# Performance work log

Measured on AMD Instinct MI355X. Metric: run time of the kernel, lower is better.

Reference implementation:

```python
import jax, jax.numpy as jnp
import numpy as np

EPS_NORM = 1e-12
BN_EPS = 1e-5
TEMP = 0.07


def _l2norm(x, axis):
    n = jnp.sqrt(jnp.sum(x * x, axis=axis, keepdims=True))
    return x / jnp.maximum(n, EPS_NORM)


def _bn_eval(z, w, b):
    # inference-mode BatchNorm2d with running_mean=0, running_var=1
    s = w / jnp.sqrt(jnp.asarray(1.0 + BN_EPS, z.dtype))
    return z * s[None, :, None, None] + b[None, :, None, None]


def setup_inputs() -> dict:
    key = jax.random.key(0)
    ks = jax.random.split(key, 8)
    B, C, H, W = 16, 256, 64, 64
    KD, P = 128, 256
    x = jax.random.normal(ks[0], (B, C, H, W), jnp.float32)
    m_features = jax.random.normal(ks[1], (P, KD), jnp.float32)
    q_w = jax.random.normal(ks[2], (KD, C), jnp.float32) * 0.05
    k_w = jax.random.normal(ks[3], (KD, KD), jnp.float32) * 0.05
    v_w = jax.random.normal(ks[4], (KD, KD), jnp.float32) * 0.05
    o_w = jax.random.normal(ks[5], (C, KD), jnp.float32) * 0.05
    dw_w = jax.random.normal(ks[6], (C, 1, 3, 3), jnp.float32) * 0.1
    return {
        "x": x, "m_features": m_features,
        "q_w": q_w, "q_b": jnp.zeros((KD,), jnp.float32),
        "k_w": k_w, "k_b": jnp.zeros((KD,), jnp.float32),
        "v_w": v_w, "v_b": jnp.zeros((KD,), jnp.float32),
        "o_w": o_w, "o_b": jnp.zeros((C,), jnp.float32),
        "dw_w": dw_w,
        "bn1_w": jnp.ones((C,), jnp.float32), "bn1_b": jnp.zeros((C,), jnp.float32),
        "bn2_w": jnp.ones((C,), jnp.float32), "bn2_b": jnp.zeros((C,), jnp.float32),
        "gamma": jnp.ones((C,), jnp.float32) * 1e-5,
    }


def reference(x, m_features, q_w, q_b, k_w, k_b, v_w, v_b, o_w, o_b,
              dw_w, bn1_w, bn1_b, bn2_w, bn2_b, gamma):
    B, C, H, W = x.shape
    KD = q_w.shape[0]
    residual = x
    # q_proj 1x1 conv -> [B,KD,H,W], L2-normalize over channel dim
    q = jnp.einsum('bchw,kc->bkhw', x, q_w) + q_b[None, :, None, None]
    q = _l2norm(q, axis=1)
    q = q.reshape(B, KD, H * W).transpose(0, 2, 1)  # [B, HW, KD]
    # k/v projections of memory bank [P, KD]
    k = _l2norm(m_features @ k_w.T + k_b, axis=-1)
    v = m_features @ v_w.T + v_b
    # fp32 attention with clamped logits
    q32, k32, v32 = q.astype(jnp.float32), k.astype(jnp.float32), v.astype(jnp.float32)
    logits = jnp.clip(jnp.einsum('bnd,pd->bnp', q32, k32) / TEMP, -30.0, 30.0)
    attn = jax.nn.softmax(logits, axis=-1)
    out = jnp.einsum('bnp,pd->bnd', attn, v32).astype(x.dtype)
    out = out.transpose(0, 2, 1).reshape(B, KD, H, W)
    # out_proj 1x1 conv -> [B,C,H,W]
    out = jnp.einsum('bkhw,ck->bchw', out, o_w) + o_b[None, :, None, None]
    # local branch: depthwise 3x3 conv + BN + exact GELU
    local = jax.lax.conv_general_dilated(
        out, dw_w, window_strides=(1, 1), padding='SAME',
        feature_group_count=C,
        dimension_numbers=('NCHW', 'OIHW', 'NCHW'))
    local = jax.nn.gelu(_bn_eval(local, bn1_w, bn1_b), approximate=False)
    out = out + local
    return _bn_eval(residual + out * gamma[None, :, None, None], bn2_w, bn2_b)
```

## Files before the change

### kernel.cpp

```cpp
#include <hip/hip_runtime.h>
#include <hip/hip_bf16.h>
#include <math.h>

#define B_ 16
#define C_ 256
#define H_ 64
#define W_ 64
#define KD_ 128
#define P_ 256
#define HW_ (H_ * W_)

typedef __bf16 bf16;
typedef bf16 bf16x8_t __attribute__((ext_vector_type(8)));
typedef bf16 bf16x4_t __attribute__((ext_vector_type(4)));
typedef float f32x4_t __attribute__((ext_vector_type(4)));
typedef float f32x16_t __attribute__((ext_vector_type(16)));
typedef unsigned char u8;

__device__ __forceinline__ unsigned cvt_pk_fp8_lo(float a, float b, unsigned old) {
#if __has_builtin(__builtin_amdgcn_cvt_pk_fp8_f32)
    return __builtin_amdgcn_cvt_pk_fp8_f32(a, b, old, false);
#else
    unsigned r = old;
    asm("v_cvt_pk_fp8_f32 %0, %1, %2" : "+v"(r) : "v"(a), "v"(b));
    return r;
#endif
}
__device__ __forceinline__ unsigned cvt_pk_fp8_hi(float a, float b, unsigned old) {
#if __has_builtin(__builtin_amdgcn_cvt_pk_fp8_f32)
    return __builtin_amdgcn_cvt_pk_fp8_f32(a, b, old, true);
#else
    unsigned r = old;
    asm("v_cvt_pk_fp8_f32 %0, %1, %2 op_sel:[0,0,1]" : "+v"(r) : "v"(a), "v"(b));
    return r;
#endif
}
__device__ __forceinline__ uint2 pack8_fp8(const float* f) {
    uint2 r;
    r.x = cvt_pk_fp8_hi(f[2], f[3], cvt_pk_fp8_lo(f[0], f[1], 0u));
    r.y = cvt_pk_fp8_hi(f[6], f[7], cvt_pk_fp8_lo(f[4], f[5], 0u));
    return r;
}

__global__ __launch_bounds__(128) void k_prep1(
    const float* __restrict__ m_feat,
    const float* __restrict__ k_w, const float* __restrict__ k_b,
    const float* __restrict__ v_w, const float* __restrict__ v_b,
    float* __restrict__ kn_f, float* __restrict__ v_f)
{
    const int p = blockIdx.x;
    const int j = threadIdx.x;
    __shared__ float msh[KD_];
    __shared__ float red[2];
    msh[j] = m_feat[p * KD_ + j];
    __syncthreads();

    float ka = k_b[j];
    float va = v_b[j];
#pragma unroll 4
    for (int d = 0; d < KD_; ++d) {
        const float m = msh[d];
        ka = fmaf(m, k_w[j * KD_ + d], ka);
        va = fmaf(m, v_w[j * KD_ + d], va);
    }
    float s = ka * ka;
#pragma unroll
    for (int o = 1; o < 64; o <<= 1) s += __shfl_xor(s, o);
    if ((j & 63) == 0) red[j >> 6] = s;
    __syncthreads();
    s = red[0] + red[1];
    const float inv = 1.0f / (0.07f * fmaxf(sqrtf(s), 1e-12f));
    kn_f[p * KD_ + j] = ka * inv;
    v_f[p * KD_ + j] = va;
}

__global__ __launch_bounds__(256) void k_prep23(
    const float* __restrict__ o_w, const float* __restrict__ v_f,
    const float* __restrict__ q_w, const float* __restrict__ kn_f,
    bf16* __restrict__ m2_bf, u8* __restrict__ qw8, u8* __restrict__ kn8)
{
    if (blockIdx.x < 256) {
        const int c = blockIdx.x;
        const int p = threadIdx.x;
        __shared__ float osh[KD_];
        if (p < KD_) osh[p] = o_w[c * KD_ + p];
        __syncthreads();
        float acc = 0.f;
#pragma unroll 4
        for (int k = 0; k < KD_; ++k) acc = fmaf(osh[k], v_f[p * KD_ + k], acc);
        const int mt = c >> 5, r = c & 31;
        const int ks = p >> 4, sub = (p >> 3) & 1, jj = p & 7;
        m2_bf[(((mt * 16 + ks) * 64) + sub * 32 + r) * 8 + jj] = (bf16)acc;
    } else {
        const int t = (blockIdx.x - 256) * 256 + threadIdx.x;
        float f[8];
        if (t < 4096) {
            const int lane = t & 63, g = t >> 6, mt = g >> 4, ks = g & 15;
            const int row = mt * 32 + (lane & 31), k0 = ks * 16 + (lane >> 5) * 8;
            const float* src = q_w + row * C_ + k0;
#pragma unroll
            for (int j = 0; j < 8; ++j) f[j] = src[j] * 16.0f;
            ((uint2*)qw8)[t] = pack8_fp8(f);
        } else {
            const int u = t - 4096;
            const int lane = u & 63, g = u >> 6, mt = g >> 3, ks = g & 7;
            const int row = mt * 32 + (lane & 31), k0 = ks * 16 + (lane >> 5) * 8;
            const float* src = kn_f + row * KD_ + k0;
#pragma unroll
            for (int j = 0; j < 8; ++j) f[j] = src[j];
            ((uint2*)kn8)[u] = pack8_fp8(f);
        }
    }
}

__global__ __launch_bounds__(512, 4) void k_attn(
    const float* __restrict__ x,
    const float* __restrict__ q_b, const float* __restrict__ o_b,
    const u8* __restrict__ qw8, const u8* __restrict__ kn8,
    const bf16* __restrict__ m2_bf, bf16* __restrict__ outf)
{
    __shared__ __align__(16) char lds[71680];
    char* const xs   = lds;
    char* const qbuf = lds + 32768;
    char* const ebuf = lds;
    float* ss_lds  = (float*)(lds + 65536);
    float* sum_lds = (float*)(lds + 67584);

    const int h0 = blockIdx.x * 2;
    const int b = blockIdx.y;
    const int tid = threadIdx.x;
    const int lane = tid & 63;
    const int wid = tid >> 6;
    const int l31 = lane & 31;
    const int kh  = lane >> 5;
    const int mtA = wid & 3, nhalf = wid >> 2;

    long kna[8];
#pragma unroll
    for (int ks = 0; ks < 8; ++ks)
        kna[ks] = *(const long*)(kn8 + ((wid * 8 + ks) * 64 + lane) * 8);

    {
        const int wq = tid & 15;
        const int cg = tid >> 4;
        const int c0 = cg * 8;
        const float* xrow = x + (size_t)b * C_ * HW_ + h0 * W_;
#pragma unroll
        for (int hl = 0; hl < 2; ++hl) {
            float v[8][4];
#pragma unroll
            for (int jj = 0; jj < 8; ++jj) {
                const f32x4_t t = *(const f32x4_t*)(xrow + (size_t)(c0 + jj) * HW_ + hl * W_ + wq * 4);
                v[jj][0] = t[0]; v[jj][1] = t[1]; v[jj][2] = t[2]; v[jj][3] = t[3];
            }
#pragma unroll
            for (int k = 0; k < 4; ++k) {
                const int pix = hl * 64 + wq * 4 + k;
                float f[8];
#pragma unroll
                for (int jj = 0; jj < 8; ++jj) f[jj] = v[jj][k];
                const int byte = pix * 256 + (c0 ^ ((pix & 31) << 3));
                *(uint2*)(xs + byte) = pack8_fp8(f);
            }
        }
    }
    __syncthreads();

    f32x16_t qacc[2];
#pragma unroll
    for (int nt = 0; nt < 2; ++nt)
#pragma unroll
        for (int i = 0; i < 16; ++i) qacc[nt][i] = 0.f;
#pragma unroll
    for (int ks = 0; ks < 16; ++ks) {
        const long a = *(const long*)(qw8 + ((mtA * 16 + ks) * 64 + lane) * 8);
#pragma unroll
        for (int nt = 0; nt < 2; ++nt) {
            const int pix = (nhalf * 2 + nt) * 32 + l31;
            const long bx = *(const long*)(xs + pix * 256 + ((ks * 16 + kh * 8) ^ (l31 << 3)));
            qacc[nt] = __builtin_amdgcn_mfma_f32_32x32x16_fp8_fp8(a, bx, qacc[nt], 0, 0, 0);
        }
    }
    {
        f32x4_t qbv[4];
#pragma unroll
        for (int g = 0; g < 4; ++g)
            qbv[g] = *(const f32x4_t*)(q_b + mtA * 32 + g * 8 + kh * 4);
#pragma unroll
        for (int nt = 0; nt < 2; ++nt) {
            const int pix = (nhalf * 2 + nt) * 32 + l31;
            float ssp = 0.f;
#pragma unroll
            for (int reg = 0; reg < 16; ++reg) {
                const int g = reg >> 2, i = reg & 3;
                const float qv = qacc[nt][reg] + 16.0f * qbv[g][i];
                qacc[nt][reg] = qv;
                ssp = fmaf(qv, qv, ssp);
            }
            ssp += __shfl_xor(ssp, 32);
            if (lane < 32) ss_lds[pix * 4 + mtA] = ssp;
#pragma unroll
            for (int g = 0; g < 4; ++g) {
                const unsigned qw_ = cvt_pk_fp8_hi(qacc[nt][g * 4 + 2], qacc[nt][g * 4 + 3],
                                    cvt_pk_fp8_lo(qacc[nt][g * 4 + 0], qacc[nt][g * 4 + 1], 0u));
                const int byte = pix * 128 + ((mtA * 32 + g * 8 + kh * 4) ^ ((l31 & 15) << 3));
                *(unsigned*)(qbuf + byte) = qw_;
            }
        }
    }
    __syncthreads();

    f32x16_t lacc[4];
#pragma unroll
    for (int nt = 0; nt < 4; ++nt)
#pragma unroll
        for (int i = 0; i < 16; ++i) lacc[nt][i] = 0.f;
#pragma unroll
    for (int ks = 0; ks < 8; ++ks) {
#pragma unroll
        for (int nt = 0; nt < 4; ++nt) {
            const int pix = nt * 32 + l31;
            const long bq = *(const long*)(qbuf + pix * 128 + ((ks * 16 + kh * 8) ^ ((l31 & 15) << 3)));
            lacc[nt] = __builtin_amdgcn_mfma_f32_32x32x16_fp8_fp8(kna[ks], bq, lacc[nt], 0, 0, 0);
        }
    }
    __syncthreads();

#pragma unroll
    for (int nt = 0; nt < 4; ++nt) {
        const int pix = nt * 32 + l31;
        const f32x4_t s4 = *(const f32x4_t*)(ss_lds + pix * 4);
        const float qinv = 1.0f / fmaxf(sqrtf(s4[0] + s4[1] + s4[2] + s4[3]), 1e-12f);
        float sm = 0.f;
#pragma unroll
        for (int reg = 0; reg < 16; ++reg) {
            const float e = __expf(lacc[nt][reg] * qinv);
            lacc[nt][reg] = e;
            sm += e;
        }
        sm += __shfl_xor(sm, 32);
        if (lane < 32) sum_lds[pix * 8 + wid] = sm;
#pragma unroll
        for (int g = 0; g < 4; ++g) {
            bf16x4_t e4;
#pragma unroll
            for (int i = 0; i < 4; ++i) e4[i] = (bf16)lacc[nt][g * 4 + i];
            const int byte = pix * 512 + (((wid * 32 + g * 8 + kh * 4) * 2) ^ (l31 << 4));
            *(bf16x4_t*)(ebuf + byte) = e4;
        }
    }
    __syncthreads();

    f32x16_t oacc[4];
#pragma unroll
    for (int nt = 0; nt < 4; ++nt)
#pragma unroll
        for (int i = 0; i < 16; ++i) oacc[nt][i] = 0.f;
#pragma unroll
    for (int ks = 0; ks < 16; ++ks) {
        const bf16x8_t a = *(const bf16x8_t*)(m2_bf + ((wid * 16 + ks) * 64 + lane) * 8);
#pragma unroll
        for (int nt = 0; nt < 4; ++nt) {
            const int pix = nt * 32 + l31;
            const bf16x8_t ba = *(const bf16x8_t*)(ebuf + pix * 512 + ((ks * 32 + kh * 16) ^ (l31 << 4)));
            oacc[nt] = __builtin_amdgcn_mfma_f32_32x32x16_bf16(a, ba, oacc[nt], 0, 0, 0);
        }
    }
    {
        f32x4_t obv[4];
#pragma unroll
        for (int g = 0; g < 4; ++g)
            obv[g] = *(const f32x4_t*)(o_b + wid * 32 + g * 8 + kh * 4);
        bf16* const obase = outf + (size_t)b * C_ * HW_ + h0 * W_;
#pragma unroll
        for (int nt = 0; nt < 4; ++nt) {
            const int pix = nt * 32 + l31;
            const f32x4_t sa = *(const f32x4_t*)(sum_lds + pix * 8);
            const f32x4_t sb = *(const f32x4_t*)(sum_lds + pix * 8 + 4);
            const float rs = 1.0f / ((sa[0] + sa[1] + sa[2] + sa[3]) +
                                     (sb[0] + sb[1] + sb[2] + sb[3]));
#pragma unroll
            for (int reg = 0; reg < 16; ++reg) {
                const int g = reg >> 2, i = reg & 3;
                const int c = wid * 32 + g * 8 + kh * 4 + i;
                obase[(size_t)c * HW_ + pix] = (bf16)fmaf(oacc[nt][reg], rs, obv[g][i]);
            }
        }
    }
}

__global__ __launch_bounds__(256) void k_post(
    const float* __restrict__ x, const bf16* __restrict__ outf,
    const float* __restrict__ dw_w,
    const float* __restrict__ bn1_w, const float* __restrict__ bn1_b,
    const float* __restrict__ bn2_w, const float* __restrict__ bn2_b,
    const float* __restrict__ gamma, float* __restrict__ y)
{
    __shared__ __align__(16) bf16 os[HW_];
    const int bc = blockIdx.x;
    const int c = bc & (C_ - 1);
    const int tid = threadIdx.x;

    const bf16* oc = outf + (size_t)bc * HW_;
#pragma unroll
    for (int it = 0; it < 2; ++it) {
        const int e = (it * 256 + tid) * 8;
        *(bf16x8_t*)&os[e] = *(const bf16x8_t*)&oc[e];
    }

    const float cbn = 0.99999500003750f;
    const float s1 = bn1_w[c] * cbn, b1 = bn1_b[c];
    const float s2 = bn2_w[c] * cbn, b2 = bn2_b[c];
    const float g = gamma[c];
    float kw[9];
#pragma unroll
    for (int j = 0; j < 9; ++j) kw[j] = dw_w[c * 9 + j];

    __syncthreads();

    const int w = tid & 63;
    const int h0 = (tid >> 6) * 16;

    float r0[3], r1[3], r2[3];
    auto ldrow = [&](int hh, float* r) {
        if ((unsigned)hh < (unsigned)H_) {
            r[1] = (float)os[hh * W_ + w];
            r[0] = (w > 0) ? (float)os[hh * W_ + w - 1] : 0.f;
            r[2] = (w < W_ - 1) ? (float)os[hh * W_ + w + 1] : 0.f;
        } else {
            r[0] = r[1] = r[2] = 0.f;
        }
    };
    ldrow(h0 - 1, r0);
    ldrow(h0, r1);

    const float* xc = x + (size_t)bc * HW_;
    float* yc = y + (size_t)bc * HW_;

#pragma unroll
    for (int i = 0; i < 16; ++i) {
        const int h = h0 + i;
        ldrow(h + 1, r2);
        float conv = kw[0] * r0[0];
        conv = fmaf(kw[1], r0[1], conv);
        conv = fmaf(kw[2], r0[2], conv);
        conv = fmaf(kw[3], r1[0], conv);
        conv = fmaf(kw[4], r1[1], conv);
        conv = fmaf(kw[5], r1[2], conv);
        conv = fmaf(kw[6], r2[0], conv);
        conv = fmaf(kw[7], r2[1], conv);
        conv = fmaf(kw[8], r2[2], conv);
        const float center = r1[1];
        const float t = fmaf(conv, s1, b1);
        const float lg = t / (1.0f + __expf(-1.702f * t));
        const int idx = h * W_ + w;
        yc[idx] = fmaf(center + lg, g, xc[idx]) * s2 + b2;
#pragma unroll
        for (int j = 0; j < 3; ++j) { r0[j] = r1[j]; r1[j] = r2[j]; }
    }
}

extern "C" void kernel_launch(void* const* d_in, const int* in_sizes, int n_in,
                              void* d_out, int out_size, void* d_ws, size_t ws_size,
                              hipStream_t stream)
{
    const float* x     = (const float*)d_in[0];
    const float* m_f   = (const float*)d_in[1];
    const float* q_w   = (const float*)d_in[2];
    const float* q_b   = (const float*)d_in[3];
    const float* k_w   = (const float*)d_in[4];
    const float* k_b   = (const float*)d_in[5];
    const float* v_w   = (const float*)d_in[6];
    const float* v_b   = (const float*)d_in[7];
    const float* o_w   = (const float*)d_in[8];
    const float* o_b   = (const float*)d_in[9];
    const float* dw_w  = (const float*)d_in[10];
    const float* bn1_w = (const float*)d_in[11];
    const float* bn1_b = (const float*)d_in[12];
    const float* bn2_w = (const float*)d_in[13];
    const float* bn2_b = (const float*)d_in[14];
    const float* gamma = (const float*)d_in[15];

    char* ws = (char*)d_ws;
    u8*    qw8   = (u8*)(ws);
    u8*    kn8   = (u8*)(ws + (32 << 10));
    bf16*  m2_bf = (bf16*)(ws + (64 << 10));
    bf16*  outf  = (bf16*)(ws + (384 << 10));
    float* kn_f  = (float*)(ws + (384 << 10));
    float* v_f   = (float*)(ws + (384 << 10) + (128 << 10));

    k_prep1<<<dim3(P_), dim3(128), 0, stream>>>(m_f, k_w, k_b, v_w, v_b,
                                                kn_f, v_f);
    k_prep23<<<dim3(288), dim3(256), 0, stream>>>(o_w, v_f, q_w, kn_f,
                                                  m2_bf, qw8, kn8);
    k_attn<<<dim3(H_ / 2, B_), dim3(512), 0, stream>>>(x, q_b, o_b, qw8, kn8,
                                                       m2_bf, outf);
    k_post<<<dim3(B_ * C_), dim3(256), 0, stream>>>(
        x, outf, dw_w, bn1_w, bn1_b, bn2_w, bn2_b, gamma, (float*)d_out);
}
```

Baseline: 75.35 us.

## Use FP8 for attention-value GEMM and halve attention tile to one row

The attention kernel now processes one image row (64 pixels) per 256-thread block instead of two rows per 512-thread block, which cuts LDS use from about 70KB to 27KB so more blocks can share a CU. The softmax probabilities and the fused o_w·v matrix are stored as FP8 (the latter scaled by 16) so the final GEMM uses FP8 MFMA instead of BF16. A per-pixel max is reduced across waves and subtracted, with a fixed offset, to keep the exponentials in FP8 range. This adds an extra barrier and reduction and lowers the precision of the attention output.

Measured after the change: 74.94 us. No clear change (-0.5%).

```diff
diff --git a/kernel.cpp b/kernel.cpp
--- a/kernel.cpp
+++ b/kernel.cpp
@@ -12,7 +12,6 @@
 
 typedef __bf16 bf16;
 typedef bf16 bf16x8_t __attribute__((ext_vector_type(8)));
-typedef bf16 bf16x4_t __attribute__((ext_vector_type(4)));
 typedef float f32x4_t __attribute__((ext_vector_type(4)));
 typedef float f32x16_t __attribute__((ext_vector_type(16)));
 typedef unsigned char u8;
@@ -77,7 +76,7 @@
 __global__ __launch_bounds__(256) void k_prep23(
     const float* __restrict__ o_w, const float* __restrict__ v_f,
     const float* __restrict__ q_w, const float* __restrict__ kn_f,
-    bf16* __restrict__ m2_bf, u8* __restrict__ qw8, u8* __restrict__ kn8)
+    u8* __restrict__ m28, u8* __restrict__ qw8, u8* __restrict__ kn8)
 {
     if (blockIdx.x < 256) {
         const int c = blockIdx.x;
@@ -90,7 +89,8 @@
         for (int k = 0; k < KD_; ++k) acc = fmaf(osh[k], v_f[p * KD_ + k], acc);
         const int mt = c >> 5, r = c & 31;
         const int ks = p >> 4, sub = (p >> 3) & 1, jj = p & 7;
-        m2_bf[(((mt * 16 + ks) * 64) + sub * 32 + r) * 8 + jj] = (bf16)acc;
+        const unsigned pk = cvt_pk_fp8_lo(acc * 16.0f, 0.f, 0u);
+        m28[(((mt * 16 + ks) * 64) + sub * 32 + r) * 8 + jj] = (u8)(pk & 0xffu);
     } else {
         const int t = (blockIdx.x - 256) * 256 + threadIdx.x;
         float f[8];
@@ -113,54 +113,48 @@
     }
 }
 
-__global__ __launch_bounds__(512, 4) void k_attn(
+__global__ __launch_bounds__(256, 4) void k_attn(
     const float* __restrict__ x,
     const float* __restrict__ q_b, const float* __restrict__ o_b,
     const u8* __restrict__ qw8, const u8* __restrict__ kn8,
-    const bf16* __restrict__ m2_bf, bf16* __restrict__ outf)
+    const u8* __restrict__ m28, bf16* __restrict__ outf)
 {
-    __shared__ __align__(16) char lds[71680];
+    __shared__ __align__(16) char lds[27648];
     char* const xs   = lds;
-    char* const qbuf = lds + 32768;
+    char* const qbuf = lds + 16384;
     char* const ebuf = lds;
-    float* ss_lds  = (float*)(lds + 65536);
-    float* sum_lds = (float*)(lds + 67584);
-
-    const int h0 = blockIdx.x * 2;
+    float* ss_lds   = (float*)(lds + 24576);
+    float* pmax_lds = (float*)(lds + 25600);
+    float* sum_lds  = (float*)(lds + 26624);
+
+    const int h = blockIdx.x;
     const int b = blockIdx.y;
     const int tid = threadIdx.x;
     const int lane = tid & 63;
     const int wid = tid >> 6;
     const int l31 = lane & 31;
     const int kh  = lane >> 5;
-    const int mtA = wid & 3, nhalf = wid >> 2;
-
-    long kna[8];
-#pragma unroll
-    for (int ks = 0; ks < 8; ++ks)
-        kna[ks] = *(const long*)(kn8 + ((wid * 8 + ks) * 64 + lane) * 8);
 
     {
         const int wq = tid & 15;
         const int cg = tid >> 4;
-        const int c0 = cg * 8;
-        const float* xrow = x + (size_t)b * C_ * HW_ + h0 * W_;
-#pragma unroll
-        for (int hl = 0; hl < 2; ++hl) {
+        const float* xrow = x + (size_t)b * C_ * HW_ + h * W_;
+#pragma unroll
+        for (int half = 0; half < 2; ++half) {
+            const int c0 = cg * 16 + half * 8;
             float v[8][4];
 #pragma unroll
             for (int jj = 0; jj < 8; ++jj) {
-                const f32x4_t t = *(const f32x4_t*)(xrow + (size_t)(c0 + jj) * HW_ + hl * W_ + wq * 4);
+                const f32x4_t t = *(const f32x4_t*)(xrow + (size_t)(c0 + jj) * HW_ + wq * 4);
                 v[jj][0] = t[0]; v[jj][1] = t[1]; v[jj][2] = t[2]; v[jj][3] = t[3];
             }
 #pragma unroll
             for (int k = 0; k < 4; ++k) {
-                const int pix = hl * 64 + wq * 4 + k;
+                const int pix = wq * 4 + k;
                 float f[8];
 #pragma unroll
                 for (int jj = 0; jj < 8; ++jj) f[jj] = v[jj][k];
-                const int byte = pix * 256 + (c0 ^ ((pix & 31) << 3));
-                *(uint2*)(xs + byte) = pack8_fp8(f);
+                *(uint2*)(xs + pix * 256 + (c0 ^ ((pix & 31) << 3))) = pack8_fp8(f);
             }
         }
     }
@@ -173,10 +167,10 @@
         for (int i = 0; i < 16; ++i) qacc[nt][i] = 0.f;
 #pragma unroll
     for (int ks = 0; ks < 16; ++ks) {
-        const long a = *(const long*)(qw8 + ((mtA * 16 + ks) * 64 + lane) * 8);
+        const long a = *(const long*)(qw8 + ((wid * 16 + ks) * 64 + lane) * 8);
 #pragma unroll
         for (int nt = 0; nt < 2; ++nt) {
-            const int pix = (nhalf * 2 + nt) * 32 + l31;
+            const int pix = nt * 32 + l31;
             const long bx = *(const long*)(xs + pix * 256 + ((ks * 16 + kh * 8) ^ (l31 << 3)));
             qacc[nt] = __builtin_amdgcn_mfma_f32_32x32x16_fp8_fp8(a, bx, qacc[nt], 0, 0, 0);
         }
@@ -185,10 +179,10 @@
         f32x4_t qbv[4];
 #pragma unroll
         for (int g = 0; g < 4; ++g)
-            qbv[g] = *(const f32x4_t*)(q_b + mtA * 32 + g * 8 + kh * 4);
+            qbv[g] = *(const f32x4_t*)(q_b + wid * 32 + g * 8 + kh * 4);
 #pragma unroll
         for (int nt = 0; nt < 2; ++nt) {
-            const int pix = (nhalf * 2 + nt) * 32 + l31;
+            const int pix = nt * 32 + l31;
             float ssp = 0.f;
 #pragma unroll
             for (int reg = 0; reg < 16; ++reg) {
@@ -198,92 +192,121 @@
                 ssp = fmaf(qv, qv, ssp);
             }
             ssp += __shfl_xor(ssp, 32);
-            if (lane < 32) ss_lds[pix * 4 + mtA] = ssp;
+            if (lane < 32) ss_lds[pix * 4 + wid] = ssp;
 #pragma unroll
             for (int g = 0; g < 4; ++g) {
                 const unsigned qw_ = cvt_pk_fp8_hi(qacc[nt][g * 4 + 2], qacc[nt][g * 4 + 3],
                                     cvt_pk_fp8_lo(qacc[nt][g * 4 + 0], qacc[nt][g * 4 + 1], 0u));
-                const int byte = pix * 128 + ((mtA * 32 + g * 8 + kh * 4) ^ ((l31 & 15) << 3));
-                *(unsigned*)(qbuf + byte) = qw_;
-            }
-        }
-    }
-    __syncthreads();
-
-    f32x16_t lacc[4];
-#pragma unroll
-    for (int nt = 0; nt < 4; ++nt)
-#pragma unroll
-        for (int i = 0; i < 16; ++i) lacc[nt][i] = 0.f;
+                *(unsigned*)(qbuf + pix * 128 +
+                             ((wid * 32 + g * 8 + kh * 4) ^ ((l31 & 15) << 3))) = qw_;
+            }
+        }
+    }
+    __syncthreads();
+
+    f32x16_t lacc[2][2];
+#pragma unroll
+    for (int m = 0; m < 2; ++m)
+#pragma unroll
+        for (int nt = 0; nt < 2; ++nt)
+#pragma unroll
+            for (int i = 0; i < 16; ++i) lacc[m][nt][i] = 0.f;
 #pragma unroll
     for (int ks = 0; ks < 8; ++ks) {
-#pragma unroll
-        for (int nt = 0; nt < 4; ++nt) {
+        const long a0 = *(const long*)(kn8 + (((wid * 2 + 0) * 8 + ks) * 64 + lane) * 8);
+        const long a1 = *(const long*)(kn8 + (((wid * 2 + 1) * 8 + ks) * 64 + lane) * 8);
+#pragma unroll
+        for (int nt = 0; nt < 2; ++nt) {
             const int pix = nt * 32 + l31;
-            const long bq = *(const long*)(qbuf + pix * 128 + ((ks * 16 + kh * 8) ^ ((l31 & 15) << 3)));
-            lacc[nt] = __builtin_amdgcn_mfma_f32_32x32x16_fp8_fp8(kna[ks], bq, lacc[nt], 0, 0, 0);
-        }
-    }
-    __syncthreads();
-
-#pragma unroll
-    for (int nt = 0; nt < 4; ++nt) {
+            const long bq = *(const long*)(qbuf + pix * 128 +
+                                           ((ks * 16 + kh * 8) ^ ((l31 & 15) << 3)));
+            lacc[0][nt] = __builtin_amdgcn_mfma_f32_32x32x16_fp8_fp8(a0, bq, lacc[0][nt], 0, 0, 0);
+            lacc[1][nt] = __builtin_amdgcn_mfma_f32_32x32x16_fp8_fp8(a1, bq, lacc[1][nt], 0, 0, 0);
+        }
+    }
+#pragma unroll
+    for (int nt = 0; nt < 2; ++nt) {
+        const int pix = nt * 32 + l31;
+        float mx = lacc[0][nt][0];
+#pragma unroll
+        for (int i = 1; i < 16; ++i) mx = fmaxf(mx, lacc[0][nt][i]);
+#pragma unroll
+        for (int i = 0; i < 16; ++i) mx = fmaxf(mx, lacc[1][nt][i]);
+        mx = fmaxf(mx, __shfl_xor(mx, 32));
+        if (lane < 32) pmax_lds[pix * 4 + wid] = mx;
+    }
+    __syncthreads();
+
+#pragma unroll
+    for (int nt = 0; nt < 2; ++nt) {
         const int pix = nt * 32 + l31;
         const f32x4_t s4 = *(const f32x4_t*)(ss_lds + pix * 4);
         const float qinv = 1.0f / fmaxf(sqrtf(s4[0] + s4[1] + s4[2] + s4[3]), 1e-12f);
+        const f32x4_t m4 = *(const f32x4_t*)(pmax_lds + pix * 4);
+        const float cof = 5.545177444479562f -
+                          fmaxf(fmaxf(m4[0], m4[1]), fmaxf(m4[2], m4[3])) * qinv;
         float sm = 0.f;
 #pragma unroll
-        for (int reg = 0; reg < 16; ++reg) {
-            const float e = __expf(lacc[nt][reg] * qinv);
-            lacc[nt][reg] = e;
-            sm += e;
+        for (int m = 0; m < 2; ++m) {
+#pragma unroll
+            for (int g = 0; g < 4; ++g) {
+                float e[4];
+#pragma unroll
+                for (int i = 0; i < 4; ++i) {
+                    e[i] = __expf(fmaf(lacc[m][nt][g * 4 + i], qinv, cof));
+                    sm += e[i];
+                }
+                const unsigned ew = cvt_pk_fp8_hi(e[2], e[3],
+                                    cvt_pk_fp8_lo(e[0], e[1], 0u));
+                const int p0 = (wid * 2 + m) * 32 + g * 8 + kh * 4;
+                *(unsigned*)(ebuf + pix * 256 + (p0 ^ (l31 << 3))) = ew;
+            }
         }
         sm += __shfl_xor(sm, 32);
-        if (lane < 32) sum_lds[pix * 8 + wid] = sm;
-#pragma unroll
-        for (int g = 0; g < 4; ++g) {
-            bf16x4_t e4;
-#pragma unroll
-            for (int i = 0; i < 4; ++i) e4[i] = (bf16)lacc[nt][g * 4 + i];
-            const int byte = pix * 512 + (((wid * 32 + g * 8 + kh * 4) * 2) ^ (l31 << 4));
-            *(bf16x4_t*)(ebuf + byte) = e4;
-        }
-    }
-    __syncthreads();
-
-    f32x16_t oacc[4];
-#pragma unroll
-    for (int nt = 0; nt < 4; ++nt)
-#pragma unroll
-        for (int i = 0; i < 16; ++i) oacc[nt][i] = 0.f;
+        if (lane < 32) sum_lds[pix * 4 + wid] = sm;
+    }
+    __syncthreads();
+
+    f32x16_t oacc[2][2];
+#pragma unroll
+    for (int m = 0; m < 2; ++m)
+#pragma unroll
+        for (int nt = 0; nt < 2; ++nt)
+#pragma unroll
+            for (int i = 0; i < 16; ++i) oacc[m][nt][i] = 0.f;
 #pragma unroll
     for (int ks = 0; ks < 16; ++ks) {
-        const bf16x8_t a = *(const bf16x8_t*)(m2_bf + ((wid * 16 + ks) * 64 + lane) * 8);
-#pragma unroll
-        for (int nt = 0; nt < 4; ++nt) {
+        const long a0 = *(const long*)(m28 + (((wid * 2 + 0) * 16 + ks) * 64 + lane) * 8);
+        const long a1 = *(const long*)(m28 + (((wid * 2 + 1) * 16 + ks) * 64 + lane) * 8);
+#pragma unroll
+        for (int nt = 0; nt < 2; ++nt) {
             const int pix = nt * 32 + l31;
-            const bf16x8_t ba = *(const bf16x8_t*)(ebuf + pix * 512 + ((ks * 32 + kh * 16) ^ (l31 << 4)));
-            oacc[nt] = __builtin_amdgcn_mfma_f32_32x32x16_bf16(a, ba, oacc[nt], 0, 0, 0);
+            const long be = *(const long*)(ebuf + pix * 256 +
+                                           ((ks * 16 + kh * 8) ^ (l31 << 3)));
+            oacc[0][nt] = __builtin_amdgcn_mfma_f32_32x32x16_fp8_fp8(a0, be, oacc[0][nt], 0, 0, 0);
+            oacc[1][nt] = __builtin_amdgcn_mfma_f32_32x32x16_fp8_fp8(a1, be, oacc[1][nt], 0, 0, 0);
         }
     }
     {
-        f32x4_t obv[4];
-#pragma unroll
-        for (int g = 0; g < 4; ++g)
-            obv[g] = *(const f32x4_t*)(o_b + wid * 32 + g * 8 + kh * 4);
-        bf16* const obase = outf + (size_t)b * C_ * HW_ + h0 * W_;
-#pragma unroll
-        for (int nt = 0; nt < 4; ++nt) {
-            const int pix = nt * 32 + l31;
-            const f32x4_t sa = *(const f32x4_t*)(sum_lds + pix * 8);
-            const f32x4_t sb = *(const f32x4_t*)(sum_lds + pix * 8 + 4);
-            const float rs = 1.0f / ((sa[0] + sa[1] + sa[2] + sa[3]) +
-                                     (sb[0] + sb[1] + sb[2] + sb[3]));
-#pragma unroll
-            for (int reg = 0; reg < 16; ++reg) {
-                const int g = reg >> 2, i = reg & 3;
-                const int c = wid * 32 + g * 8 + kh * 4 + i;
-                obase[(size_t)c * HW_ + pix] = (bf16)fmaf(oacc[nt][reg], rs, obv[g][i]);
+        bf16* const obase = outf + (size_t)b * C_ * HW_ + h * W_;
+#pragma unroll
+        for (int m = 0; m < 2; ++m) {
+            const int cw = (wid * 2 + m) * 32;
+            f32x4_t obv[4];
+#pragma unroll
+            for (int g = 0; g < 4; ++g)
+                obv[g] = *(const f32x4_t*)(o_b + cw + g * 8 + kh * 4);
+#pragma unroll
+            for (int nt = 0; nt < 2; ++nt) {
+                const int pix = nt * 32 + l31;
+                const f32x4_t sv = *(const f32x4_t*)(sum_lds + pix * 4);
+                const float rs = 1.0f / (16.0f * (sv[0] + sv[1] + sv[2] + sv[3]));
+#pragma unroll
+                for (int reg = 0; reg < 16; ++reg) {
+                    const int g = reg >> 2, i = reg & 3;
+                    const int c = cw + g * 8 + kh * 4 + i;
+                    obase[(size_t)c * HW_ + pix] = (bf16)fmaf(oacc[m][nt][reg], rs, obv[g][i]);
+                }
             }
         }
     }
@@ -384,7 +407,7 @@
     char* ws = (char*)d_ws;
     u8*    qw8   = (u8*)(ws);
     u8*    kn8   = (u8*)(ws + (32 << 10));
-    bf16*  m2_bf = (bf16*)(ws + (64 << 10));
+    u8*    m28   = (u8*)(ws + (64 << 10));
     bf16*  outf  = (bf16*)(ws + (384 << 10));
     float* kn_f  = (float*)(ws + (384 << 10));
     float* v_f   = (float*)(ws + (384 << 10) + (128 << 10));
@@ -392,9 +415,9 @@
     k_prep1<<<dim3(P_), dim3(128), 0, stream>>>(m_f, k_w, k_b, v_w, v_b,
                                                 kn_f, v_f);
     k_prep23<<<dim3(288), dim3(256), 0, stream>>>(o_w, v_f, q_w, kn_f,
-                                                  m2_bf, qw8, kn8);
-    k_attn<<<dim3(H_ / 2, B_), dim3(512), 0, stream>>>(x, q_b, o_b, qw8, kn8,
-                                                       m2_bf, outf);
+                                                  m28, qw8, kn8);
+    k_attn<<<dim3(H_, B_), dim3(256), 0, stream>>>(x, q_b, o_b, qw8, kn8,
+                                                   m28, outf);
     k_post<<<dim3(B_ * C_), dim3(256), 0, stream>>>(
         x, outf, dw_w, bn1_w, bn1_b, bn2_w, bn2_b, gamma, (float*)d_out);
 }
```
